# Kernel tuning notes

Hardware: AMD Instinct MI355X
Metric: run time of the kernel (lower is better)

Reference implementation:

```python
import jax, jax.numpy as jnp
import numpy as np

BANDWIDTH = 1.0
EPS = 1e-20


def setup_inputs() -> dict:
    key = jax.random.key(0)
    k1, k2, k3 = jax.random.split(key, 3)
    test_X = jax.random.normal(k1, (8192, 64), dtype=jnp.float32)
    train_X = jax.random.normal(k2, (16384, 64), dtype=jnp.float32)
    sample_weight = jax.random.uniform(k3, (16384,), dtype=jnp.float32)
    return {"test_X": test_X, "train_X": train_X, "sample_weight": sample_weight}


def reference(test_X, train_X, sample_weight):
    # test_X: [m, d], train_X: [n, d], sample_weight: [n]
    d = train_X.shape[1]
    h = jnp.float32(BANDWIDTH)
    # weights are normalized; with weights, n is treated as 1 => log(n) = 0
    w = sample_weight / jnp.sum(sample_weight)
    Z = 0.5 * d * jnp.log(2.0 * jnp.float32(np.pi)) + d * jnp.log(h)
    # squared L2 distances via expansion (avoids [m, n, d] intermediate)
    t2 = jnp.sum(test_X * test_X, axis=-1)  # [m]
    r2 = jnp.sum(train_X * train_X, axis=-1)  # [n]
    cross = test_X @ train_X.T  # [m, n]
    sq = (t2[:, None] + r2[None, :] - 2.0 * cross) / (h * h)  # [m, n]
    val = -0.5 * sq - Z  # [m, n]
    # weighted, numerically-stable log-sum-exp over train dim
    m_max = jnp.max(val, axis=-1, keepdims=True)  # [m, 1]
    s = jnp.sum(jnp.exp(val - m_max) * w[None, :], axis=-1)  # [m]
    return m_max[:, 0] + jnp.log(s + EPS)
```

## Files before the change

### kernel.cpp

```cpp
#include <hip/hip_runtime.h>
#include <hip/hip_bf16.h>
#include <math.h>

#define M 8192
#define N 16384
#define D 64
#define ZC 58.81206612509905f
#define B0 24.0f
#define LOG2E 1.4426950408889634f
#define HL2E 0.7213475204444817f
#define LN2 0.6931471805599453f

#define PCH 32
#define NCHK (N / PCH)

typedef short v8bf __attribute__((ext_vector_type(8)));
typedef float v16f __attribute__((ext_vector_type(16)));

#define B_AU2  0
#define B_LW2  32768
#define B_PART 98304
#define B_TB   1146880
#define B_TR   2195456

__global__ __launch_bounds__(256) void gk_prep(const float* __restrict__ testX,
                                               const float* __restrict__ trainX,
                                               const float* __restrict__ sw,
                                               __hip_bfloat16* __restrict__ tb,
                                               __hip_bfloat16* __restrict__ rb,
                                               float* __restrict__ au2,
                                               float* __restrict__ lw2) {
    const int tid = threadIdx.x;
    const int e = tid & 7;
    if (blockIdx.x < M / 32) {
        const int row = blockIdx.x * 32 + (tid >> 3);
        const float4* p = reinterpret_cast<const float4*>(testX + (size_t)row * D + e * 8);
        float4 v0 = p[0], v1 = p[1];
        float t2 = v0.x * v0.x + v0.y * v0.y + v0.z * v0.z + v0.w * v0.w
                 + v1.x * v1.x + v1.y * v1.y + v1.z * v1.z + v1.w * v1.w;
        t2 += __shfl_xor(t2, 1, 64);
        t2 += __shfl_xor(t2, 2, 64);
        t2 += __shfl_xor(t2, 4, 64);
        if (e == 0) au2[row] = -HL2E * t2;
        union { __hip_bfloat16 h[8]; uint4 u; } cv;
        cv.h[0] = __float2bfloat16(v0.x * LOG2E);
        cv.h[1] = __float2bfloat16(v0.y * LOG2E);
        cv.h[2] = __float2bfloat16(v0.z * LOG2E);
        cv.h[3] = __float2bfloat16(v0.w * LOG2E);
        cv.h[4] = __float2bfloat16(v1.x * LOG2E);
        cv.h[5] = __float2bfloat16(v1.y * LOG2E);
        cv.h[6] = __float2bfloat16(v1.z * LOG2E);
        cv.h[7] = __float2bfloat16(v1.w * LOG2E);
        *reinterpret_cast<uint4*>(tb + (size_t)row * D + e * 8) = cv.u;
    } else {
        const int row = (blockIdx.x - M / 32) * 32 + (tid >> 3);
        const float4* p = reinterpret_cast<const float4*>(trainX + (size_t)row * D + e * 8);
        float4 v0 = p[0], v1 = p[1];
        float r2 = v0.x * v0.x + v0.y * v0.y + v0.z * v0.z + v0.w * v0.w
                 + v1.x * v1.x + v1.y * v1.y + v1.z * v1.z + v1.w * v1.w;
        r2 += __shfl_xor(r2, 1, 64);
        r2 += __shfl_xor(r2, 2, 64);
        r2 += __shfl_xor(r2, 4, 64);
        if (e == 0) lw2[row] = __builtin_amdgcn_logf(sw[row]) - HL2E * r2 + B0;
        union { __hip_bfloat16 h[8]; uint4 u; } cv;
        cv.h[0] = __float2bfloat16(v0.x);
        cv.h[1] = __float2bfloat16(v0.y);
        cv.h[2] = __float2bfloat16(v0.z);
        cv.h[3] = __float2bfloat16(v0.w);
        cv.h[4] = __float2bfloat16(v1.x);
        cv.h[5] = __float2bfloat16(v1.y);
        cv.h[6] = __float2bfloat16(v1.z);
        cv.h[7] = __float2bfloat16(v1.w);
        *reinterpret_cast<uint4*>(rb + (size_t)row * D + e * 8) = cv.u;
    }
}

__global__ __launch_bounds__(256, 4) void gk_main(const __hip_bfloat16* __restrict__ ta,
                                                  const __hip_bfloat16* __restrict__ tr,
                                                  const float* __restrict__ lw2,
                                                  float* __restrict__ part) {
    __shared__ __align__(16) char smem[17408];
    const int tid = threadIdx.x;
    const int w = tid >> 6;
    const int lane = tid & 63;
    const int c = lane & 31;
    const int h = lane >> 5;
    const int rl = lane >> 3;
    const int kb = lane & 7;

    const int bid = blockIdx.x;
    const int xcd = bid & 7;
    const int j = bid >> 3;
    const int chunk = xcd * 4 + (j & 3);
    const int m0 = (j >> 2) * 128;
    const int n0 = chunk * NCHK;

    const __hip_bfloat16* arow = ta + (size_t)(m0 + w * 32 + c) * D;
    v8bf af[4];
#pragma unroll
    for (int t = 0; t < 4; ++t)
        af[t] = *reinterpret_cast<const v8bf*>(arow + (2 * t + h) * 8);

    float srun[16];
#pragma unroll
    for (int r = 0; r < 16; ++r) srun[r] = 0.f;

    char* Bs = smem;
    float* Lw = reinterpret_cast<float*>(smem + 16384);

    for (int tile = 0; tile < NCHK / 128; ++tile) {
        __syncthreads();
        const int nt0 = n0 + tile * 128;
#pragma unroll
        for (int i = 0; i < 4; ++i) {
            int rr = w * 32 + i * 8 + rl;
            uint4 v = *reinterpret_cast<const uint4*>(tr + (size_t)(nt0 + rr) * D + kb * 8);
            *reinterpret_cast<uint4*>(Bs + kb * 2048 + ((rr ^ kb) * 16)) = v;
        }
        if (tid < 128) Lw[tid] = lw2[nt0 + tid];
        __syncthreads();

#pragma unroll
        for (int s = 0; s < 4; ++s) {
            float lwv = Lw[s * 32 + c];
            v16f acc;
#pragma unroll
            for (int r = 0; r < 16; ++r) acc[r] = lwv;
#pragma unroll
            for (int t = 0; t < 4; ++t) {
                int kk = 2 * t + h;
                v8bf bf = *reinterpret_cast<const v8bf*>(Bs + kk * 2048 + (((s * 32 + c) ^ kk) * 16));
                acc = __builtin_amdgcn_mfma_f32_32x32x16_bf16(af[t], bf, acc, 0, 0, 0);
            }
#pragma unroll
            for (int r = 0; r < 16; ++r)
                srun[r] += __builtin_amdgcn_exp2f(acc[r]);
        }
    }

    __syncthreads();
    float* red = reinterpret_cast<float*>(smem);
#pragma unroll
    for (int r = 0; r < 16; ++r) {
        int rowl = (r & 3) + 8 * (r >> 2) + 4 * h;
        red[(w * 32 + rowl) * 33 + c] = srun[r];
    }
    __syncthreads();
    if (tid < 128) {
        float G = 0.f;
#pragma unroll
        for (int c2 = 0; c2 < 32; ++c2) G += red[tid * 33 + c2];
        part[(size_t)chunk * M + m0 + tid] = G;
    }
}

__global__ __launch_bounds__(256) void gk_merge(const float* __restrict__ part,
                                                const float* __restrict__ au2,
                                                const float* __restrict__ sw,
                                                float* __restrict__ out) {
    __shared__ float red[256];
    const int tid = threadIdx.x;
    float s = 0.f;
    const float4* p4 = reinterpret_cast<const float4*>(sw);
    for (int i = tid; i < N / 4; i += 256) {
        float4 v = p4[i];
        s += v.x + v.y + v.z + v.w;
    }
    red[tid] = s;
    __syncthreads();
    for (int off = 128; off > 0; off >>= 1) {
        if (tid < off) red[tid] += red[tid + off];
        __syncthreads();
    }
    const float W = red[0];

    const int r = blockIdx.x * 256 + tid;
    float G = 0.f;
#pragma unroll
    for (int p = 0; p < PCH; ++p) G += part[(size_t)p * M + r];
    out[r] = LN2 * (au2[r] + __builtin_amdgcn_logf(fmaxf(G, 1e-30f)) - B0
                   - __builtin_amdgcn_logf(W)) - ZC;
}

extern "C" void kernel_launch(void* const* d_in, const int* in_sizes, int n_in,
                              void* d_out, int out_size, void* d_ws, size_t ws_size,
                              hipStream_t stream) {
    const float* testX  = (const float*)d_in[0];
    const float* trainX = (const float*)d_in[1];
    const float* sw     = (const float*)d_in[2];
    float* out = (float*)d_out;
    char* wsb = (char*)d_ws;

    float* au2  = (float*)(wsb + B_AU2);
    float* lw2  = (float*)(wsb + B_LW2);
    float* part = (float*)(wsb + B_PART);
    __hip_bfloat16* tb = (__hip_bfloat16*)(wsb + B_TB);
    __hip_bfloat16* rb = (__hip_bfloat16*)(wsb + B_TR);

    gk_prep<<<M / 32 + N / 32, 256, 0, stream>>>(testX, trainX, sw, tb, rb, au2, lw2);
    gk_main<<<(M / 128) * PCH, 256, 0, stream>>>(tb, rb, lw2, part);
    gk_merge<<<M / 256, 256, 0, stream>>>(part, au2, sw, out);
}
```

Measured before the change: 101.5 us.

## Replace LDS-staged B tiles with direct register loads and 2x2 wave tiling

Drops the shared-memory staging of train tiles and the per-tile barriers. Each wave now loads its own B fragments straight from global memory into registers and covers a 64x256 sub-tile: two A row-blocks share each loaded B fragment, and the four waves split the block as 2 M-halves by 2 N-halves. The partial sums are combined through a larger LDS reduction buffer at the end. This removes the synchronisation and LDS traffic, at the cost of more global/L2 load traffic for B and more registers per thread, which can lower occupancy.

```diff
diff --git a/kernel.cpp b/kernel.cpp
--- a/kernel.cpp
+++ b/kernel.cpp
@@ -79,14 +79,14 @@
                                                   const __hip_bfloat16* __restrict__ tr,
                                                   const float* __restrict__ lw2,
                                                   float* __restrict__ part) {
-    __shared__ __align__(16) char smem[17408];
+    __shared__ float red[128 * 65];
     const int tid = threadIdx.x;
     const int w = tid >> 6;
     const int lane = tid & 63;
     const int c = lane & 31;
     const int h = lane >> 5;
-    const int rl = lane >> 3;
-    const int kb = lane & 7;
+    const int mhalf = w & 1;
+    const int chalf = w >> 1;
 
     const int bid = blockIdx.x;
     const int xcd = bid & 7;
@@ -95,61 +95,54 @@
     const int m0 = (j >> 2) * 128;
     const int n0 = chunk * NCHK;
 
-    const __hip_bfloat16* arow = ta + (size_t)(m0 + w * 32 + c) * D;
-    v8bf af[4];
+    v8bf af[2][4];
+    const __hip_bfloat16* ar = ta + (size_t)(m0 + mhalf * 64 + c) * D;
 #pragma unroll
-    for (int t = 0; t < 4; ++t)
-        af[t] = *reinterpret_cast<const v8bf*>(arow + (2 * t + h) * 8);
+    for (int t = 0; t < 4; ++t) {
+        af[0][t] = *reinterpret_cast<const v8bf*>(ar + (2 * t + h) * 8);
+        af[1][t] = *reinterpret_cast<const v8bf*>(ar + 32 * D + (2 * t + h) * 8);
+    }
 
-    float srun[16];
+    float srun[2][16];
 #pragma unroll
-    for (int r = 0; r < 16; ++r) srun[r] = 0.f;
+    for (int ms = 0; ms < 2; ++ms)
+#pragma unroll
+        for (int r = 0; r < 16; ++r) srun[ms][r] = 0.f;
 
-    char* Bs = smem;
-    float* Lw = reinterpret_cast<float*>(smem + 16384);
-
-    for (int tile = 0; tile < NCHK / 128; ++tile) {
-        __syncthreads();
-        const int nt0 = n0 + tile * 128;
+    for (int jt = 0; jt < 8; ++jt) {
+        const int nt = n0 + chalf * 256 + jt * 32;
+        const float lwv = lw2[nt + c];
+        const __hip_bfloat16* br = tr + (size_t)(nt + c) * D;
+        v8bf bf[4];
 #pragma unroll
-        for (int i = 0; i < 4; ++i) {
-            int rr = w * 32 + i * 8 + rl;
-            uint4 v = *reinterpret_cast<const uint4*>(tr + (size_t)(nt0 + rr) * D + kb * 8);
-            *reinterpret_cast<uint4*>(Bs + kb * 2048 + ((rr ^ kb) * 16)) = v;
-        }
-        if (tid < 128) Lw[tid] = lw2[nt0 + tid];
-        __syncthreads();
-
+        for (int t = 0; t < 4; ++t)
+            bf[t] = *reinterpret_cast<const v8bf*>(br + (2 * t + h) * 8);
 #pragma unroll
-        for (int s = 0; s < 4; ++s) {
-            float lwv = Lw[s * 32 + c];
+        for (int ms = 0; ms < 2; ++ms) {
             v16f acc;
 #pragma unroll
             for (int r = 0; r < 16; ++r) acc[r] = lwv;
 #pragma unroll
-            for (int t = 0; t < 4; ++t) {
-                int kk = 2 * t + h;
-                v8bf bf = *reinterpret_cast<const v8bf*>(Bs + kk * 2048 + (((s * 32 + c) ^ kk) * 16));
-                acc = __builtin_amdgcn_mfma_f32_32x32x16_bf16(af[t], bf, acc, 0, 0, 0);
-            }
+            for (int t = 0; t < 4; ++t)
+                acc = __builtin_amdgcn_mfma_f32_32x32x16_bf16(af[ms][t], bf[t], acc, 0, 0, 0);
 #pragma unroll
             for (int r = 0; r < 16; ++r)
-                srun[r] += __builtin_amdgcn_exp2f(acc[r]);
+                srun[ms][r] += __builtin_amdgcn_exp2f(acc[r]);
         }
     }
 
-    __syncthreads();
-    float* red = reinterpret_cast<float*>(smem);
 #pragma unroll
-    for (int r = 0; r < 16; ++r) {
-        int rowl = (r & 3) + 8 * (r >> 2) + 4 * h;
-        red[(w * 32 + rowl) * 33 + c] = srun[r];
-    }
+    for (int ms = 0; ms < 2; ++ms)
+#pragma unroll
+        for (int r = 0; r < 16; ++r) {
+            int row = mhalf * 64 + ms * 32 + (r & 3) + 8 * (r >> 2) + 4 * h;
+            red[row * 65 + chalf * 32 + c] = srun[ms][r];
+        }
     __syncthreads();
     if (tid < 128) {
         float G = 0.f;
 #pragma unroll
-        for (int c2 = 0; c2 < 32; ++c2) G += red[tid * 33 + c2];
+        for (int c2 = 0; c2 < 64; ++c2) G += red[tid * 65 + c2];
         part[(size_t)chunk * M + m0 + tid] = G;
     }
 }
```

New measurement: 109.6 us. +8.0%, slower.

## Double-buffer train tiles with direct global-to-LDS loads in main kernel

Applied to the files above, without the earlier changes.

The main kernel now loads each 128-row train tile straight into LDS with global_load_lds, skipping the round trip through registers, and alternates between two LDS buffers. The next tile is prefetched while the current one is computed. The four-tile loop is fully unrolled. The log-weight terms are read straight from global memory instead of being staged in LDS, and the XOR-swizzled layout is replaced by a grouped layout that matches the DMA write pattern. LDS use per block roughly doubles, which may limit occupancy. Correctness depends on the barriers waiting for the asynchronous LDS writes to finish.

```diff
diff --git a/kernel.cpp b/kernel.cpp
--- a/kernel.cpp
+++ b/kernel.cpp
@@ -75,18 +75,55 @@
     }
 }
 
+__device__ __forceinline__ void dma16(const void* g, void* l) {
+    __builtin_amdgcn_global_load_lds(
+        (const __attribute__((address_space(1))) unsigned int*)g,
+        (__attribute__((address_space(3))) unsigned int*)l, 16, 0, 0);
+}
+
+__device__ __forceinline__ void dma_tile(const __hip_bfloat16* tr, int nt,
+                                         char* Bsb, int w, int lane) {
+#pragma unroll
+    for (int i = 0; i < 4; ++i) {
+        const int g = w * 4 + i;
+        const __hip_bfloat16* gp =
+            tr + (size_t)(nt + g * 8 + (lane & 7)) * D + (lane >> 3) * 8;
+        dma16(gp, Bsb + g * 1024);
+    }
+}
+
+__device__ __forceinline__ void compute_tile(const char* Bs,
+                                             const float* __restrict__ lwp,
+                                             const v8bf af[4], float srun[16],
+                                             int c, int h) {
+#pragma unroll
+    for (int s = 0; s < 4; ++s) {
+        const float lwv = lwp[s * 32 + c];
+        v16f acc;
+#pragma unroll
+        for (int r = 0; r < 16; ++r) acc[r] = lwv;
+#pragma unroll
+        for (int t = 0; t < 4; ++t) {
+            const v8bf bf = *reinterpret_cast<const v8bf*>(
+                Bs + (s * 4 + (c >> 3)) * 1024 + (2 * t + h) * 128 + (c & 7) * 16);
+            acc = __builtin_amdgcn_mfma_f32_32x32x16_bf16(af[t], bf, acc, 0, 0, 0);
+        }
+#pragma unroll
+        for (int r = 0; r < 16; ++r)
+            srun[r] += __builtin_amdgcn_exp2f(acc[r]);
+    }
+}
+
 __global__ __launch_bounds__(256, 4) void gk_main(const __hip_bfloat16* __restrict__ ta,
                                                   const __hip_bfloat16* __restrict__ tr,
                                                   const float* __restrict__ lw2,
                                                   float* __restrict__ part) {
-    __shared__ __align__(16) char smem[17408];
+    __shared__ __align__(16) char smem[32768];
     const int tid = threadIdx.x;
     const int w = tid >> 6;
     const int lane = tid & 63;
     const int c = lane & 31;
     const int h = lane >> 5;
-    const int rl = lane >> 3;
-    const int kb = lane & 7;
 
     const int bid = blockIdx.x;
     const int xcd = bid & 7;
@@ -95,6 +132,11 @@
     const int m0 = (j >> 2) * 128;
     const int n0 = chunk * NCHK;
 
+    char* const Bs0 = smem;
+    char* const Bs1 = smem + 16384;
+
+    dma_tile(tr, n0, Bs0, w, lane);
+
     const __hip_bfloat16* arow = ta + (size_t)(m0 + w * 32 + c) * D;
     v8bf af[4];
 #pragma unroll
@@ -105,38 +147,17 @@
 #pragma unroll
     for (int r = 0; r < 16; ++r) srun[r] = 0.f;
 
-    char* Bs = smem;
-    float* Lw = reinterpret_cast<float*>(smem + 16384);
-
-    for (int tile = 0; tile < NCHK / 128; ++tile) {
-        __syncthreads();
-        const int nt0 = n0 + tile * 128;
-#pragma unroll
-        for (int i = 0; i < 4; ++i) {
-            int rr = w * 32 + i * 8 + rl;
-            uint4 v = *reinterpret_cast<const uint4*>(tr + (size_t)(nt0 + rr) * D + kb * 8);
-            *reinterpret_cast<uint4*>(Bs + kb * 2048 + ((rr ^ kb) * 16)) = v;
-        }
-        if (tid < 128) Lw[tid] = lw2[nt0 + tid];
-        __syncthreads();
-
-#pragma unroll
-        for (int s = 0; s < 4; ++s) {
-            float lwv = Lw[s * 32 + c];
-            v16f acc;
-#pragma unroll
-            for (int r = 0; r < 16; ++r) acc[r] = lwv;
-#pragma unroll
-            for (int t = 0; t < 4; ++t) {
-                int kk = 2 * t + h;
-                v8bf bf = *reinterpret_cast<const v8bf*>(Bs + kk * 2048 + (((s * 32 + c) ^ kk) * 16));
-                acc = __builtin_amdgcn_mfma_f32_32x32x16_bf16(af[t], bf, acc, 0, 0, 0);
-            }
-#pragma unroll
-            for (int r = 0; r < 16; ++r)
-                srun[r] += __builtin_amdgcn_exp2f(acc[r]);
-        }
-    }
+    __syncthreads();
+    dma_tile(tr, n0 + 128, Bs1, w, lane);
+    compute_tile(Bs0, lw2 + n0, af, srun, c, h);
+    __syncthreads();
+    dma_tile(tr, n0 + 256, Bs0, w, lane);
+    compute_tile(Bs1, lw2 + n0 + 128, af, srun, c, h);
+    __syncthreads();
+    dma_tile(tr, n0 + 384, Bs1, w, lane);
+    compute_tile(Bs0, lw2 + n0 + 256, af, srun, c, h);
+    __syncthreads();
+    compute_tile(Bs1, lw2 + n0 + 384, af, srun, c, h);
 
     __syncthreads();
     float* red = reinterpret_cast<float*>(smem);
```

New measurement: 100.5 us. About the same (-0.9%).
